# Optimization experiments

Measured on AMD Instinct MI355X. Metric: run time of the kernel, lower is better.

## Reference

```python
import jax, jax.numpy as jnp
import numpy as np

B = 64      # graphs per batch
N = 1024    # nodes per graph (equal-size graphs -> static top-k)
D = 256     # in_dim
DEG = 16    # avg degree
K = 512     # k = ratio * N, ratio = 0.5
E = B * N * DEG
NT = B * N


def setup_inputs() -> dict:
    key = jax.random.key(0)
    ks = jax.random.split(key, 8)
    feature = jax.random.normal(ks[0], (NT, D), jnp.float32)
    gid = jnp.repeat(jnp.arange(B), N * DEG)          # graph id per edge
    src = gid * N + jax.random.randint(ks[1], (E,), 0, N)
    dst = gid * N + jax.random.randint(ks[2], (E,), 0, N)
    label = jax.random.randint(ks[3], (B,), 0, 2)
    W = jax.random.normal(ks[4], (D, 1), jnp.float32) / np.sqrt(D)   # GraphConv weight
    b = jnp.zeros((1,), jnp.float32)                                  # GraphConv bias
    lin1_w = jax.random.normal(ks[5], (2, 1), jnp.float32) / np.sqrt(2.0)
    lin1_b = jnp.zeros((1,), jnp.float32)
    return dict(feature=feature, src=src, dst=dst, label=label,
                W=W, b=b, lin1_w=lin1_w, lin1_b=lin1_b)


def reference(feature, src, dst, label, W, b, lin1_w, lin1_b):
    fdt = feature.dtype
    # ---- get_bias_score: distance-to-class-center score ----
    node_label = jnp.repeat(label, N).astype(fdt)                 # [NT]
    gemb = feature.reshape(B, N, D).mean(axis=1)                  # AvgPooling per graph [B, D]
    lab_f = label.astype(fdt)                                     # [B]
    n1 = jnp.maximum(lab_f.sum(), 1.0)
    n0 = jnp.maximum((1.0 - lab_f).sum(), 1.0)
    center0 = (gemb * (1.0 - lab_f)[:, None]).sum(0) / n0         # [D]
    center1 = (gemb * lab_f[:, None]).sum(0) / n1                 # [D]
    d0 = jnp.sqrt(((feature - center0) ** 2).sum(-1))             # [NT]
    d1 = jnp.sqrt(((feature - center1) ** 2).sum(-1))             # [NT]
    score_distance = (d0 - d1) * ((node_label - 0.5) * 2.0)       # [NT]
    # ---- GraphConv(in_dim, 1), norm='both' (DGL semantics) ----
    ones_e = jnp.ones((E,), fdt)
    deg_out = jax.ops.segment_sum(ones_e, src, NT)
    deg_in = jax.ops.segment_sum(ones_e, dst, NT)
    ns = jnp.maximum(deg_out, 1.0) ** -0.5                        # src-side norm
    nd = jnp.maximum(deg_in, 1.0) ** -0.5                         # dst-side norm
    h = (feature @ W) * ns[:, None]                               # project first (out<in) [NT,1]
    agg = jax.ops.segment_sum(h[src], dst, NT)                    # [NT,1]
    score_gcn = (agg * nd[:, None] + b)[:, 0]                     # [NT]
    # ---- combine two scores with lin1: Linear(2, 1) ----
    score = jnp.stack([score_gcn, score_distance], axis=-1) @ lin1_w + lin1_b  # [NT,1]
    sflat = score[:, 0]
    # ---- per-graph top-k (mytopk with equal-size graphs -> static k) ----
    _, idx = jax.lax.top_k(sflat.reshape(B, N), K)                # [B,K] local indices
    perm = (idx + (jnp.arange(B) * N)[:, None]).reshape(-1)       # [B*K] global indices
    mask = jnp.ones((NT,), bool).at[perm].set(False)
    perm_com = jnp.nonzero(mask, size=NT - B * K)[0]              # complement, static size
    # ---- gather + tanh-gated features ----
    feature_dis = feature[perm] * jnp.tanh(sflat[perm])[:, None]          # [B*K, D]
    feature_com = feature[perm_com] * jnp.tanh(sflat[perm_com])[:, None]  # [B*(N-K), D]
    score_soft = jax.nn.softmax(score, axis=0)                    # softmax over all nodes
    return feature_dis, feature_com, perm, perm_com, score_soft
```

## Files before the change

kernel.cpp:

```cpp
#include <hip/hip_runtime.h>
#include <math.h>

#define Bg   64
#define Nn   1024
#define Dd   256
#define EPG  16384
#define NT   (Bg * Nn)
#define Kk   512

#define OFF_DIS   0
#define OFF_COM   8388608
#define OFF_PERM  16777216
#define OFF_PCOM  16809984
#define OFF_SOFT  16842752

#define WS_H0     0
#define WS_SFLAT  (NT * 4)
#define WS_GPART  (NT * 4 * 2)
#define WS_REDM   (WS_GPART + 1024 * 256 * 4)
#define WS_REDS   (WS_REDM + 256)
#define WS_C0     (WS_REDS + 256)
#define WS_C1     (WS_C0 + 1024)
#define WS_PERMI  (WS_C1 + 1024)
#define WS_PCOMI  (WS_PERMI + 32768 * 4)
#define WS_SGCN   (WS_PCOMI + 32768 * 4)

__global__ __launch_bounds__(256) void k_col(
        const float* __restrict__ f, const float* __restrict__ W,
        float* __restrict__ gpart, float* __restrict__ h0) {
    __shared__ float4 scol4[1024];
    int blk = blockIdx.x, t = threadIdx.x;
    int gid = t >> 4, sub = t & 15;
    int base = blk * 64 + gid * 4;
    const float4* f4 = (const float4*)f;
    const float4* W4 = (const float4*)W;
    float4 w[4];
    #pragma unroll
    for (int it = 0; it < 4; ++it) w[it] = W4[it * 16 + sub];
    float4 cs[4];
    #pragma unroll
    for (int it = 0; it < 4; ++it) cs[it] = make_float4(0.f, 0.f, 0.f, 0.f);
    float4 v[4][4];
    #pragma unroll
    for (int k = 0; k < 4; ++k) {
        size_t bofs = (size_t)(base + k) * 64;
        #pragma unroll
        for (int it = 0; it < 4; ++it) v[k][it] = f4[bofs + it * 16 + sub];
    }
    #pragma unroll
    for (int k = 0; k < 4; ++k) {
        float d = 0.f;
        #pragma unroll
        for (int it = 0; it < 4; ++it) {
            cs[it].x += v[k][it].x; cs[it].y += v[k][it].y;
            cs[it].z += v[k][it].z; cs[it].w += v[k][it].w;
            d += v[k][it].x * w[it].x + v[k][it].y * w[it].y
               + v[k][it].z * w[it].z + v[k][it].w * w[it].w;
        }
        #pragma unroll
        for (int o = 1; o < 16; o <<= 1) d += __shfl_xor(d, o);
        if (sub == 0) h0[base + k] = d;
    }
    #pragma unroll
    for (int it = 0; it < 4; ++it) scol4[gid * 64 + it * 16 + sub] = cs[it];
    __syncthreads();
    if (t < 64) {
        float4 s = make_float4(0.f, 0.f, 0.f, 0.f);
        #pragma unroll
        for (int g2 = 0; g2 < 16; ++g2) {
            float4 u = scol4[g2 * 64 + t];
            s.x += u.x; s.y += u.y; s.z += u.z; s.w += u.w;
        }
        ((float4*)(gpart + blk * Dd))[t] = s;
    }
}

__global__ __launch_bounds__(1024) void k_edge(
        const int* __restrict__ src, const int* __restrict__ dst,
        const int* __restrict__ label, const float* __restrict__ h0,
        const float* __restrict__ gpart, const float* __restrict__ b,
        float* __restrict__ sgcn, float* __restrict__ c0, float* __restrict__ c1) {
    __shared__ uint4 ep4[4096];
    __shared__ int   sdo[1024];
    __shared__ int   sdi[1024];
    __shared__ float shn[1024];
    __shared__ float ssc[1024];
    __shared__ float sc0[1024];
    __shared__ float sc1[1024];

    int g = blockIdx.x, t = threadIdx.x;
    sdo[t] = 0; sdi[t] = 0;

    if (g == 0) {
        int col = t & 255, chunk = t >> 8;
        float a0 = 0.f, a1 = 0.f;
        for (int gg = chunk * 16; gg < chunk * 16 + 16; ++gg) {
            float v = 0.f;
            #pragma unroll
            for (int p = 0; p < 16; ++p) v += gpart[(gg * 16 + p) * Dd + col];
            if (label[gg]) a1 += v; else a0 += v;
        }
        sc0[t] = a0; sc1[t] = a1;
        __syncthreads();
        if (t < Dd) {
            int n1 = 0;
            for (int gg = 0; gg < Bg; ++gg) n1 += label[gg];
            float fn1 = fmaxf((float)n1, 1.f);
            float fn0 = fmaxf((float)(Bg - n1), 1.f);
            float s0 = sc0[t] + sc0[256 + t] + sc0[512 + t] + sc0[768 + t];
            float s1 = sc1[t] + sc1[256 + t] + sc1[512 + t] + sc1[768 + t];
            c0[t] = s0 * (1.f / (float)Nn) / fn0;
            c1[t] = s1 * (1.f / (float)Nn) / fn1;
        }
    }
    __syncthreads();

    {
        const int4* s4 = (const int4*)(src + g * EPG);
        const int4* d4 = (const int4*)(dst + g * EPG);
        #pragma unroll
        for (int i = t; i < EPG / 4; i += 1024) {
            int4 ss = s4[i];
            int4 dd = d4[i];
            int s0 = ss.x & (Nn - 1), s1 = ss.y & (Nn - 1), s2 = ss.z & (Nn - 1), s3 = ss.w & (Nn - 1);
            int e0 = dd.x & (Nn - 1), e1 = dd.y & (Nn - 1), e2 = dd.z & (Nn - 1), e3 = dd.w & (Nn - 1);
            uint4 pk;
            pk.x = (unsigned)(s0 | (e0 << 16));
            pk.y = (unsigned)(s1 | (e1 << 16));
            pk.z = (unsigned)(s2 | (e2 << 16));
            pk.w = (unsigned)(s3 | (e3 << 16));
            ep4[i] = pk;
            atomicAdd(&sdo[s0], 1); atomicAdd(&sdo[s1], 1);
            atomicAdd(&sdo[s2], 1); atomicAdd(&sdo[s3], 1);
            atomicAdd(&sdi[e0], 1); atomicAdd(&sdi[e1], 1);
            atomicAdd(&sdi[e2], 1); atomicAdd(&sdi[e3], 1);
        }
    }
    __syncthreads();

    {
        int dg = sdo[t]; if (dg < 1) dg = 1;
        shn[t] = h0[g * Nn + t] / sqrtf((float)dg);
        ssc[t] = 0.f;
    }
    __syncthreads();

    #pragma unroll
    for (int i = t; i < EPG / 4; i += 1024) {
        uint4 pk = ep4[i];
        atomicAdd(&ssc[pk.x >> 16], shn[pk.x & 0xFFFF]);
        atomicAdd(&ssc[pk.y >> 16], shn[pk.y & 0xFFFF]);
        atomicAdd(&ssc[pk.z >> 16], shn[pk.z & 0xFFFF]);
        atomicAdd(&ssc[pk.w >> 16], shn[pk.w & 0xFFFF]);
    }
    __syncthreads();

    {
        int dg = sdi[t]; if (dg < 1) dg = 1;
        sgcn[g * Nn + t] = ssc[t] / sqrtf((float)dg) + b[0];
    }
}

__global__ __launch_bounds__(256) void k_score(
        const float* __restrict__ f, const float* __restrict__ c0,
        const float* __restrict__ c1, const float* __restrict__ sgcn,
        const int* __restrict__ label, const float* __restrict__ lw,
        const float* __restrict__ lb, float* __restrict__ sflat) {
    int t = threadIdx.x;
    int gid = t >> 4, sub = t & 15;
    int row0 = blockIdx.x * 32 + gid * 2;
    int g = row0 >> 10;
    const float4* f4 = (const float4*)f;
    float4 c0r[4], c1r[4];
    #pragma unroll
    for (int it = 0; it < 4; ++it) {
        c0r[it] = ((const float4*)c0)[it * 16 + sub];
        c1r[it] = ((const float4*)c1)[it * 16 + sub];
    }
    float sgn = label[g] ? 1.f : -1.f;
    float lw0 = lw[0], lw1 = lw[1], lb0 = lb[0];
    float4 v[2][4];
    #pragma unroll
    for (int r = 0; r < 2; ++r) {
        size_t bofs = (size_t)(row0 + r) * 64;
        #pragma unroll
        for (int it = 0; it < 4; ++it) v[r][it] = f4[bofs + it * 16 + sub];
    }
    #pragma unroll
    for (int r = 0; r < 2; ++r) {
        float a0 = 0.f, a1 = 0.f;
        #pragma unroll
        for (int it = 0; it < 4; ++it) {
            float dx;
            dx = v[r][it].x - c0r[it].x; a0 += dx * dx;
            dx = v[r][it].y - c0r[it].y; a0 += dx * dx;
            dx = v[r][it].z - c0r[it].z; a0 += dx * dx;
            dx = v[r][it].w - c0r[it].w; a0 += dx * dx;
            dx = v[r][it].x - c1r[it].x; a1 += dx * dx;
            dx = v[r][it].y - c1r[it].y; a1 += dx * dx;
            dx = v[r][it].z - c1r[it].z; a1 += dx * dx;
            dx = v[r][it].w - c1r[it].w; a1 += dx * dx;
        }
        #pragma unroll
        for (int o = 1; o < 16; o <<= 1) {
            a0 += __shfl_xor(a0, o);
            a1 += __shfl_xor(a1, o);
        }
        if (sub == 0) {
            int row = row0 + r;
            float sdist = (sqrtf(a0) - sqrtf(a1)) * sgn;
            sflat[row] = sgcn[row] * lw0 + sdist * lw1 + lb0;
        }
    }
}

__global__ __launch_bounds__(512) void k_topk(
        const float* __restrict__ sflat, int* __restrict__ permI,
        int* __restrict__ pcomI, float* __restrict__ out,
        float* __restrict__ redM, float* __restrict__ redS) {
    __shared__ unsigned long long sk[1024];
    __shared__ int   sflag[1024];
    __shared__ int   swave[8];
    __shared__ float sred[16];
    int g = blockIdx.x, t = threadIdx.x;
    int lane = t & 63, w = t >> 6;
    float v0 = sflat[g * Nn + t];
    float v1 = sflat[g * Nn + t + 512];
    unsigned u0 = __float_as_uint(v0);
    unsigned u1 = __float_as_uint(v1);
    unsigned o0 = u0 ^ ((u0 >> 31) ? 0xFFFFFFFFu : 0x80000000u);
    unsigned o1 = u1 ^ ((u1 >> 31) ? 0xFFFFFFFFu : 0x80000000u);
    sk[t]       = ((unsigned long long)o0 << 32) | (unsigned)(1023 - t);
    sk[t + 512] = ((unsigned long long)o1 << 32) | (unsigned)(1023 - (t + 512));
    __syncthreads();
    for (int k = 2; k <= 1024; k <<= 1) {
        for (int j = k >> 1; j > 0; j >>= 1) {
            int l = ((t & ~(j - 1)) << 1) | (t & (j - 1));
            int r = l | j;
            unsigned long long a = sk[l], bk = sk[r];
            bool up = ((l & k) == 0);
            if ((a < bk) == up) { sk[l] = bk; sk[r] = a; }
            __syncthreads();
        }
    }
    sflag[t] = 1; sflag[t + 512] = 1;
    __syncthreads();
    {
        int loc = 1023 - (int)(sk[t] & 0xFFFFFFFFu);
        sflag[loc] = 0;
        int gi = g * Nn + loc;
        permI[g * Kk + t] = gi;
        out[OFF_PERM + g * Kk + t] = (float)gi;
    }
    __syncthreads();
    int f0 = sflag[2 * t], f1 = sflag[2 * t + 1];
    int f2 = f0 + f1;
    int inc = f2;
    for (int o = 1; o < 64; o <<= 1) {
        int y = __shfl_up(inc, o);
        if (lane >= o) inc += y;
    }
    if (lane == 63) swave[w] = inc;
    __syncthreads();
    if (t < 8) {
        int a = swave[t];
        for (int o = 1; o < 8; o <<= 1) {
            int y = __shfl_up(a, o);
            if (t >= o) a += y;
        }
        swave[t] = a;
    }
    __syncthreads();
    int basep = ((w > 0) ? swave[w - 1] : 0) + (inc - f2);
    if (f0) {
        int gi = g * Nn + 2 * t;
        pcomI[g * Kk + basep] = gi;
        out[OFF_PCOM + g * Kk + basep] = (float)gi;
    }
    if (f1) {
        int pos = basep + f0;
        int gi = g * Nn + 2 * t + 1;
        pcomI[g * Kk + pos] = gi;
        out[OFF_PCOM + g * Kk + pos] = (float)gi;
    }
    float m = fmaxf(v0, v1);
    for (int o = 32; o > 0; o >>= 1) m = fmaxf(m, __shfl_xor(m, o));
    if (lane == 0) sred[w] = m;
    __syncthreads();
    if (t < 8) {
        float a = sred[t];
        for (int o = 4; o > 0; o >>= 1) a = fmaxf(a, __shfl_xor(a, o));
        if (t == 0) sred[0] = a;
    }
    __syncthreads();
    m = sred[0];
    float s = expf(v0 - m) + expf(v1 - m);
    for (int o = 32; o > 0; o >>= 1) s += __shfl_xor(s, o);
    if (lane == 0) sred[8 + w] = s;
    __syncthreads();
    if (t < 8) {
        float a = sred[8 + t];
        for (int o = 4; o > 0; o >>= 1) a += __shfl_xor(a, o);
        if (t == 0) { redM[g] = m; redS[g] = a; }
    }
}

__global__ __launch_bounds__(256) void k_write(
        const float* __restrict__ f, const int* __restrict__ permI,
        const int* __restrict__ pcomI, const float* __restrict__ sflat,
        const float* __restrict__ redM, const float* __restrict__ redS,
        float* __restrict__ out) {
    __shared__ float sMS[2];
    int t = threadIdx.x;
    if (t < 64) {
        float m = redM[t];
        float mm = m;
        for (int o = 32; o > 0; o >>= 1) mm = fmaxf(mm, __shfl_xor(mm, o));
        float s = redS[t] * expf(m - mm);
        for (int o = 32; o > 0; o >>= 1) s += __shfl_xor(s, o);
        if (t == 0) { sMS[0] = mm; sMS[1] = s; }
    }
    __syncthreads();
    float M = sMS[0], S = sMS[1];
    if (t < 16) {
        int i = blockIdx.x * 16 + t;
        out[OFF_SOFT + i] = expf(sflat[i] - M) / S;
    }
    int w = t >> 6, lane = t & 63;
    int j0 = blockIdx.x * 16 + w * 4;
    int rows[4];
    float tv[4];
    #pragma unroll
    for (int i = 0; i < 4; ++i) {
        int j = j0 + i;
        rows[i] = (j < 32768) ? permI[j] : pcomI[j - 32768];
    }
    #pragma unroll
    for (int i = 0; i < 4; ++i) tv[i] = tanhf(sflat[rows[i]]);
    const float4* f4 = (const float4*)f;
    float4* o4 = (float4*)out;
    #pragma unroll
    for (int i = 0; i < 4; ++i) {
        float4 v = f4[(size_t)rows[i] * 64 + lane];
        o4[(size_t)(j0 + i) * 64 + lane] =
            make_float4(v.x * tv[i], v.y * tv[i], v.z * tv[i], v.w * tv[i]);
    }
}

extern "C" void kernel_launch(void* const* d_in, const int* in_sizes, int n_in,
                              void* d_out, int out_size, void* d_ws, size_t ws_size,
                              hipStream_t stream) {
    const float* feature = (const float*)d_in[0];
    const int*   src     = (const int*)d_in[1];
    const int*   dst     = (const int*)d_in[2];
    const int*   label   = (const int*)d_in[3];
    const float* W       = (const float*)d_in[4];
    const float* b       = (const float*)d_in[5];
    const float* lw      = (const float*)d_in[6];
    const float* lb      = (const float*)d_in[7];
    float* out = (float*)d_out;
    char*  ws  = (char*)d_ws;

    float* h0    = (float*)(ws + WS_H0);
    float* sflat = (float*)(ws + WS_SFLAT);
    float* gpart = (float*)(ws + WS_GPART);
    float* redM  = (float*)(ws + WS_REDM);
    float* redS  = (float*)(ws + WS_REDS);
    float* c0    = (float*)(ws + WS_C0);
    float* c1    = (float*)(ws + WS_C1);
    int*   permI = (int*)(ws + WS_PERMI);
    int*   pcomI = (int*)(ws + WS_PCOMI);
    float* sgcn  = (float*)(ws + WS_SGCN);

    k_col  <<<1024, 256,  0, stream>>>(feature, W, gpart, h0);
    k_edge <<<Bg,   1024, 0, stream>>>(src, dst, label, h0, gpart, b, sgcn, c0, c1);
    k_score<<<2048, 256,  0, stream>>>(feature, c0, c1, sgcn, label, lw, lb, sflat);
    k_topk <<<Bg,   512,  0, stream>>>(sflat, permI, pcomI, out, redM, redS);
    k_write<<<4096, 256,  0, stream>>>(feature, permI, pcomI, sflat, redM, redS, out);
}
```

Measured before the change: 201.9 us.

## Fuse all five stages into one cooperative persistent kernel with grid syncs

Replaces the five separate kernel launches with a single cooperative kernel of 256 blocks of 1024 threads, using grid.sync between the column-sum/projection, edge aggregation, scoring, top-k and gather phases. Each block now handles more rows per phase, and the top-k bitonic sort runs with 512 active threads out of 1024. This aims to remove launch gaps and inter-kernel drain. In exchange it adds grid-wide barrier costs, leaves most blocks idle in the 64-block phases, and relies on a large LDS allocation per block.

```diff
diff --git a/kernel.cpp b/kernel.cpp
--- a/kernel.cpp
+++ b/kernel.cpp
@@ -1,5 +1,8 @@
 #include <hip/hip_runtime.h>
+#include <hip/hip_cooperative_groups.h>
 #include <math.h>
+
+namespace cg = cooperative_groups;
 
 #define Bg   64
 #define Nn   1024
@@ -25,79 +28,135 @@
 #define WS_PCOMI  (WS_PERMI + 32768 * 4)
 #define WS_SGCN   (WS_PCOMI + 32768 * 4)
 
-__global__ __launch_bounds__(256) void k_col(
+__global__ __launch_bounds__(1024) void k_fused(
         const float* __restrict__ f, const float* __restrict__ W,
-        float* __restrict__ gpart, float* __restrict__ h0) {
-    __shared__ float4 scol4[1024];
+        const int* __restrict__ src, const int* __restrict__ dst,
+        const int* __restrict__ label, const float* __restrict__ b,
+        const float* __restrict__ lw, const float* __restrict__ lb,
+        float* __restrict__ h0, float* __restrict__ gpart,
+        float* __restrict__ c0, float* __restrict__ c1,
+        float* __restrict__ sgcn, float* __restrict__ sflat,
+        int* __restrict__ permI, int* __restrict__ pcomI,
+        float* __restrict__ redM, float* __restrict__ redS,
+        float* __restrict__ out) {
+    __shared__ alignas(16) char smem[81920];
+    __shared__ int   swave[8];
+    __shared__ float sred[33];
+    __shared__ float sMS[2];
+
+    cg::grid_group grid = cg::this_grid();
     int blk = blockIdx.x, t = threadIdx.x;
-    int gid = t >> 4, sub = t & 15;
-    int base = blk * 64 + gid * 4;
-    const float4* f4 = (const float4*)f;
-    const float4* W4 = (const float4*)W;
-    float4 w[4];
-    #pragma unroll
-    for (int it = 0; it < 4; ++it) w[it] = W4[it * 16 + sub];
-    float4 cs[4];
-    #pragma unroll
-    for (int it = 0; it < 4; ++it) cs[it] = make_float4(0.f, 0.f, 0.f, 0.f);
-    float4 v[4][4];
-    #pragma unroll
-    for (int k = 0; k < 4; ++k) {
-        size_t bofs = (size_t)(base + k) * 64;
-        #pragma unroll
-        for (int it = 0; it < 4; ++it) v[k][it] = f4[bofs + it * 16 + sub];
-    }
-    #pragma unroll
-    for (int k = 0; k < 4; ++k) {
-        float d = 0.f;
-        #pragma unroll
-        for (int it = 0; it < 4; ++it) {
-            cs[it].x += v[k][it].x; cs[it].y += v[k][it].y;
-            cs[it].z += v[k][it].z; cs[it].w += v[k][it].w;
-            d += v[k][it].x * w[it].x + v[k][it].y * w[it].y
-               + v[k][it].z * w[it].z + v[k][it].w * w[it].w;
-        }
-        #pragma unroll
-        for (int o = 1; o < 16; o <<= 1) d += __shfl_xor(d, o);
-        if (sub == 0) h0[base + k] = d;
-    }
-    #pragma unroll
-    for (int it = 0; it < 4; ++it) scol4[gid * 64 + it * 16 + sub] = cs[it];
-    __syncthreads();
-    if (t < 64) {
-        float4 s = make_float4(0.f, 0.f, 0.f, 0.f);
-        #pragma unroll
-        for (int g2 = 0; g2 < 16; ++g2) {
-            float4 u = scol4[g2 * 64 + t];
-            s.x += u.x; s.y += u.y; s.z += u.z; s.w += u.w;
-        }
-        ((float4*)(gpart + blk * Dd))[t] = s;
-    }
-}
-
-__global__ __launch_bounds__(1024) void k_edge(
-        const int* __restrict__ src, const int* __restrict__ dst,
-        const int* __restrict__ label, const float* __restrict__ h0,
-        const float* __restrict__ gpart, const float* __restrict__ b,
-        float* __restrict__ sgcn, float* __restrict__ c0, float* __restrict__ c1) {
-    __shared__ uint4 ep4[4096];
-    __shared__ int   sdo[1024];
-    __shared__ int   sdi[1024];
-    __shared__ float shn[1024];
-    __shared__ float ssc[1024];
-    __shared__ float sc0[1024];
-    __shared__ float sc1[1024];
-
-    int g = blockIdx.x, t = threadIdx.x;
-    sdo[t] = 0; sdi[t] = 0;
-
-    if (g == 0) {
+
+    {
+        float4* scol4 = (float4*)smem;
+        int gid = t >> 4, sub = t & 15;
+        int base = blk * 256 + gid * 4;
+        const float4* f4 = (const float4*)f;
+        const float4* W4 = (const float4*)W;
+        float4 w[4];
+        #pragma unroll
+        for (int it = 0; it < 4; ++it) w[it] = W4[it * 16 + sub];
+        float4 cs[4];
+        #pragma unroll
+        for (int it = 0; it < 4; ++it) cs[it] = make_float4(0.f, 0.f, 0.f, 0.f);
+        #pragma unroll
+        for (int kb = 0; kb < 2; ++kb) {
+            float4 v[2][4];
+            #pragma unroll
+            for (int k = 0; k < 2; ++k) {
+                size_t bofs = (size_t)(base + kb * 2 + k) * 64;
+                #pragma unroll
+                for (int it = 0; it < 4; ++it) v[k][it] = f4[bofs + it * 16 + sub];
+            }
+            #pragma unroll
+            for (int k = 0; k < 2; ++k) {
+                float d = 0.f;
+                #pragma unroll
+                for (int it = 0; it < 4; ++it) {
+                    cs[it].x += v[k][it].x; cs[it].y += v[k][it].y;
+                    cs[it].z += v[k][it].z; cs[it].w += v[k][it].w;
+                    d += v[k][it].x * w[it].x + v[k][it].y * w[it].y
+                       + v[k][it].z * w[it].z + v[k][it].w * w[it].w;
+                }
+                #pragma unroll
+                for (int o = 1; o < 16; o <<= 1) d += __shfl_xor(d, o);
+                if (sub == 0) h0[base + kb * 2 + k] = d;
+            }
+        }
+        #pragma unroll
+        for (int it = 0; it < 4; ++it) scol4[gid * 64 + it * 16 + sub] = cs[it];
+        __syncthreads();
+        if (t < 256) {
+            float4 s = make_float4(0.f, 0.f, 0.f, 0.f);
+            #pragma unroll
+            for (int g2 = 0; g2 < 64; ++g2) {
+                float4 u = scol4[g2 * 64 + t];
+                s.x += u.x; s.y += u.y; s.z += u.z; s.w += u.w;
+            }
+            ((float4*)gpart)[blk * 64 + t] = s;
+        }
+    }
+    grid.sync();
+
+    if (blk < 64) {
+        uint4* ep4 = (uint4*)smem;
+        int*   sdo = (int*)(smem + 65536);
+        int*   sdi = (int*)(smem + 69632);
+        float* shn = (float*)(smem + 73728);
+        float* ssc = (float*)(smem + 77824);
+        int g = blk;
+        sdo[t] = 0; sdi[t] = 0;
+        __syncthreads();
+        {
+            const int4* s4 = (const int4*)(src + g * EPG);
+            const int4* d4 = (const int4*)(dst + g * EPG);
+            #pragma unroll
+            for (int i = t; i < EPG / 4; i += 1024) {
+                int4 ss = s4[i];
+                int4 dd = d4[i];
+                int s0 = ss.x & (Nn - 1), s1 = ss.y & (Nn - 1), s2 = ss.z & (Nn - 1), s3 = ss.w & (Nn - 1);
+                int e0 = dd.x & (Nn - 1), e1 = dd.y & (Nn - 1), e2 = dd.z & (Nn - 1), e3 = dd.w & (Nn - 1);
+                uint4 pk;
+                pk.x = (unsigned)(s0 | (e0 << 16));
+                pk.y = (unsigned)(s1 | (e1 << 16));
+                pk.z = (unsigned)(s2 | (e2 << 16));
+                pk.w = (unsigned)(s3 | (e3 << 16));
+                ep4[i] = pk;
+                atomicAdd(&sdo[s0], 1); atomicAdd(&sdo[s1], 1);
+                atomicAdd(&sdo[s2], 1); atomicAdd(&sdo[s3], 1);
+                atomicAdd(&sdi[e0], 1); atomicAdd(&sdi[e1], 1);
+                atomicAdd(&sdi[e2], 1); atomicAdd(&sdi[e3], 1);
+            }
+        }
+        __syncthreads();
+        {
+            int dg = sdo[t]; if (dg < 1) dg = 1;
+            shn[t] = h0[g * Nn + t] / sqrtf((float)dg);
+            ssc[t] = 0.f;
+        }
+        __syncthreads();
+        #pragma unroll
+        for (int i = t; i < EPG / 4; i += 1024) {
+            uint4 pk = ep4[i];
+            atomicAdd(&ssc[pk.x >> 16], shn[pk.x & 0xFFFF]);
+            atomicAdd(&ssc[pk.y >> 16], shn[pk.y & 0xFFFF]);
+            atomicAdd(&ssc[pk.z >> 16], shn[pk.z & 0xFFFF]);
+            atomicAdd(&ssc[pk.w >> 16], shn[pk.w & 0xFFFF]);
+        }
+        __syncthreads();
+        {
+            int dg = sdi[t]; if (dg < 1) dg = 1;
+            sgcn[g * Nn + t] = ssc[t] / sqrtf((float)dg) + b[0];
+        }
+    } else if (blk == 64) {
+        float* sc0 = (float*)smem;
+        float* sc1 = (float*)(smem + 4096);
         int col = t & 255, chunk = t >> 8;
         float a0 = 0.f, a1 = 0.f;
         for (int gg = chunk * 16; gg < chunk * 16 + 16; ++gg) {
             float v = 0.f;
             #pragma unroll
-            for (int p = 0; p < 16; ++p) v += gpart[(gg * 16 + p) * Dd + col];
+            for (int p = 0; p < 4; ++p) v += gpart[(gg * 4 + p) * Dd + col];
             if (label[gg]) a1 += v; else a0 += v;
         }
         sc0[t] = a0; sc1[t] = a1;
@@ -113,237 +172,188 @@
             c1[t] = s1 * (1.f / (float)Nn) / fn1;
         }
     }
-    __syncthreads();
+    grid.sync();
 
     {
-        const int4* s4 = (const int4*)(src + g * EPG);
-        const int4* d4 = (const int4*)(dst + g * EPG);
-        #pragma unroll
-        for (int i = t; i < EPG / 4; i += 1024) {
-            int4 ss = s4[i];
-            int4 dd = d4[i];
-            int s0 = ss.x & (Nn - 1), s1 = ss.y & (Nn - 1), s2 = ss.z & (Nn - 1), s3 = ss.w & (Nn - 1);
-            int e0 = dd.x & (Nn - 1), e1 = dd.y & (Nn - 1), e2 = dd.z & (Nn - 1), e3 = dd.w & (Nn - 1);
-            uint4 pk;
-            pk.x = (unsigned)(s0 | (e0 << 16));
-            pk.y = (unsigned)(s1 | (e1 << 16));
-            pk.z = (unsigned)(s2 | (e2 << 16));
-            pk.w = (unsigned)(s3 | (e3 << 16));
-            ep4[i] = pk;
-            atomicAdd(&sdo[s0], 1); atomicAdd(&sdo[s1], 1);
-            atomicAdd(&sdo[s2], 1); atomicAdd(&sdo[s3], 1);
-            atomicAdd(&sdi[e0], 1); atomicAdd(&sdi[e1], 1);
-            atomicAdd(&sdi[e2], 1); atomicAdd(&sdi[e3], 1);
-        }
-    }
-    __syncthreads();
+        int gid = t >> 4, sub = t & 15;
+        int row0 = blk * 256 + gid * 4;
+        int g = row0 >> 10;
+        const float4* f4 = (const float4*)f;
+        float4 c0r[4], c1r[4];
+        #pragma unroll
+        for (int it = 0; it < 4; ++it) {
+            c0r[it] = ((const float4*)c0)[it * 16 + sub];
+            c1r[it] = ((const float4*)c1)[it * 16 + sub];
+        }
+        float sgn = label[g] ? 1.f : -1.f;
+        float lw0 = lw[0], lw1 = lw[1], lb0 = lb[0];
+        #pragma unroll
+        for (int rb = 0; rb < 2; ++rb) {
+            float4 v[2][4];
+            #pragma unroll
+            for (int r = 0; r < 2; ++r) {
+                size_t bofs = (size_t)(row0 + rb * 2 + r) * 64;
+                #pragma unroll
+                for (int it = 0; it < 4; ++it) v[r][it] = f4[bofs + it * 16 + sub];
+            }
+            #pragma unroll
+            for (int r = 0; r < 2; ++r) {
+                float a0 = 0.f, a1 = 0.f;
+                #pragma unroll
+                for (int it = 0; it < 4; ++it) {
+                    float dx;
+                    dx = v[r][it].x - c0r[it].x; a0 += dx * dx;
+                    dx = v[r][it].y - c0r[it].y; a0 += dx * dx;
+                    dx = v[r][it].z - c0r[it].z; a0 += dx * dx;
+                    dx = v[r][it].w - c0r[it].w; a0 += dx * dx;
+                    dx = v[r][it].x - c1r[it].x; a1 += dx * dx;
+                    dx = v[r][it].y - c1r[it].y; a1 += dx * dx;
+                    dx = v[r][it].z - c1r[it].z; a1 += dx * dx;
+                    dx = v[r][it].w - c1r[it].w; a1 += dx * dx;
+                }
+                #pragma unroll
+                for (int o = 1; o < 16; o <<= 1) {
+                    a0 += __shfl_xor(a0, o);
+                    a1 += __shfl_xor(a1, o);
+                }
+                if (sub == 0) {
+                    int row = row0 + rb * 2 + r;
+                    float sdist = (sqrtf(a0) - sqrtf(a1)) * sgn;
+                    sflat[row] = sgcn[row] * lw0 + sdist * lw1 + lb0;
+                }
+            }
+        }
+    }
+    grid.sync();
+
+    if (blk < 64) {
+        unsigned long long* sk = (unsigned long long*)smem;
+        int* sflag = (int*)(smem + 8192);
+        int g = blk;
+        int lane = t & 63, w16 = t >> 6;
+        float v = sflat[g * Nn + t];
+        {
+            unsigned u = __float_as_uint(v);
+            unsigned ox = u ^ ((u >> 31) ? 0xFFFFFFFFu : 0x80000000u);
+            sk[t] = ((unsigned long long)ox << 32) | (unsigned)(1023 - t);
+        }
+        __syncthreads();
+        for (int k = 2; k <= 1024; k <<= 1) {
+            for (int j = k >> 1; j > 0; j >>= 1) {
+                if (t < 512) {
+                    int l = ((t & ~(j - 1)) << 1) | (t & (j - 1));
+                    int r = l | j;
+                    unsigned long long A = sk[l], Bk = sk[r];
+                    bool up = ((l & k) == 0);
+                    if ((A < Bk) == up) { sk[l] = Bk; sk[r] = A; }
+                }
+                __syncthreads();
+            }
+        }
+        sflag[t] = 1;
+        __syncthreads();
+        if (t < 512) {
+            int loc = 1023 - (int)(sk[t] & 0xFFFFFFFFu);
+            sflag[loc] = 0;
+            int gi = g * Nn + loc;
+            permI[g * Kk + t] = gi;
+            out[OFF_PERM + g * Kk + t] = (float)gi;
+        }
+        __syncthreads();
+        int f0 = 0, f1 = 0, f2 = 0, inc = 0;
+        if (t < 512) {
+            f0 = sflag[2 * t]; f1 = sflag[2 * t + 1];
+            f2 = f0 + f1; inc = f2;
+            for (int o = 1; o < 64; o <<= 1) {
+                int y = __shfl_up(inc, o);
+                if (lane >= o) inc += y;
+            }
+            if (lane == 63) swave[w16] = inc;
+        }
+        __syncthreads();
+        if (t < 8) {
+            int a = swave[t];
+            for (int o = 1; o < 8; o <<= 1) {
+                int y = __shfl_up(a, o);
+                if (t >= o) a += y;
+            }
+            swave[t] = a;
+        }
+        __syncthreads();
+        if (t < 512) {
+            int basep = ((w16 > 0) ? swave[w16 - 1] : 0) + (inc - f2);
+            if (f0) {
+                int gi = g * Nn + 2 * t;
+                pcomI[g * Kk + basep] = gi;
+                out[OFF_PCOM + g * Kk + basep] = (float)gi;
+            }
+            if (f1) {
+                int pos = basep + f0;
+                int gi = g * Nn + 2 * t + 1;
+                pcomI[g * Kk + pos] = gi;
+                out[OFF_PCOM + g * Kk + pos] = (float)gi;
+            }
+        }
+        float m = v;
+        for (int o = 32; o > 0; o >>= 1) m = fmaxf(m, __shfl_xor(m, o));
+        if (lane == 0) sred[w16] = m;
+        __syncthreads();
+        if (t < 16) {
+            float a = sred[t];
+            for (int o = 8; o > 0; o >>= 1) a = fmaxf(a, __shfl_xor(a, o));
+            if (t == 0) sred[32] = a;
+        }
+        __syncthreads();
+        float M = sred[32];
+        float s = expf(v - M);
+        for (int o = 32; o > 0; o >>= 1) s += __shfl_xor(s, o);
+        if (lane == 0) sred[16 + w16] = s;
+        __syncthreads();
+        if (t < 16) {
+            float a = sred[16 + t];
+            for (int o = 8; o > 0; o >>= 1) a += __shfl_xor(a, o);
+            if (t == 0) { redM[g] = M; redS[g] = a; }
+        }
+    }
+    grid.sync();
 
     {
-        int dg = sdo[t]; if (dg < 1) dg = 1;
-        shn[t] = h0[g * Nn + t] / sqrtf((float)dg);
-        ssc[t] = 0.f;
-    }
-    __syncthreads();
-
-    #pragma unroll
-    for (int i = t; i < EPG / 4; i += 1024) {
-        uint4 pk = ep4[i];
-        atomicAdd(&ssc[pk.x >> 16], shn[pk.x & 0xFFFF]);
-        atomicAdd(&ssc[pk.y >> 16], shn[pk.y & 0xFFFF]);
-        atomicAdd(&ssc[pk.z >> 16], shn[pk.z & 0xFFFF]);
-        atomicAdd(&ssc[pk.w >> 16], shn[pk.w & 0xFFFF]);
-    }
-    __syncthreads();
-
-    {
-        int dg = sdi[t]; if (dg < 1) dg = 1;
-        sgcn[g * Nn + t] = ssc[t] / sqrtf((float)dg) + b[0];
-    }
-}
-
-__global__ __launch_bounds__(256) void k_score(
-        const float* __restrict__ f, const float* __restrict__ c0,
-        const float* __restrict__ c1, const float* __restrict__ sgcn,
-        const int* __restrict__ label, const float* __restrict__ lw,
-        const float* __restrict__ lb, float* __restrict__ sflat) {
-    int t = threadIdx.x;
-    int gid = t >> 4, sub = t & 15;
-    int row0 = blockIdx.x * 32 + gid * 2;
-    int g = row0 >> 10;
-    const float4* f4 = (const float4*)f;
-    float4 c0r[4], c1r[4];
-    #pragma unroll
-    for (int it = 0; it < 4; ++it) {
-        c0r[it] = ((const float4*)c0)[it * 16 + sub];
-        c1r[it] = ((const float4*)c1)[it * 16 + sub];
-    }
-    float sgn = label[g] ? 1.f : -1.f;
-    float lw0 = lw[0], lw1 = lw[1], lb0 = lb[0];
-    float4 v[2][4];
-    #pragma unroll
-    for (int r = 0; r < 2; ++r) {
-        size_t bofs = (size_t)(row0 + r) * 64;
-        #pragma unroll
-        for (int it = 0; it < 4; ++it) v[r][it] = f4[bofs + it * 16 + sub];
-    }
-    #pragma unroll
-    for (int r = 0; r < 2; ++r) {
-        float a0 = 0.f, a1 = 0.f;
-        #pragma unroll
-        for (int it = 0; it < 4; ++it) {
-            float dx;
-            dx = v[r][it].x - c0r[it].x; a0 += dx * dx;
-            dx = v[r][it].y - c0r[it].y; a0 += dx * dx;
-            dx = v[r][it].z - c0r[it].z; a0 += dx * dx;
-            dx = v[r][it].w - c0r[it].w; a0 += dx * dx;
-            dx = v[r][it].x - c1r[it].x; a1 += dx * dx;
-            dx = v[r][it].y - c1r[it].y; a1 += dx * dx;
-            dx = v[r][it].z - c1r[it].z; a1 += dx * dx;
-            dx = v[r][it].w - c1r[it].w; a1 += dx * dx;
-        }
-        #pragma unroll
-        for (int o = 1; o < 16; o <<= 1) {
-            a0 += __shfl_xor(a0, o);
-            a1 += __shfl_xor(a1, o);
-        }
-        if (sub == 0) {
-            int row = row0 + r;
-            float sdist = (sqrtf(a0) - sqrtf(a1)) * sgn;
-            sflat[row] = sgcn[row] * lw0 + sdist * lw1 + lb0;
-        }
-    }
-}
-
-__global__ __launch_bounds__(512) void k_topk(
-        const float* __restrict__ sflat, int* __restrict__ permI,
-        int* __restrict__ pcomI, float* __restrict__ out,
-        float* __restrict__ redM, float* __restrict__ redS) {
-    __shared__ unsigned long long sk[1024];
-    __shared__ int   sflag[1024];
-    __shared__ int   swave[8];
-    __shared__ float sred[16];
-    int g = blockIdx.x, t = threadIdx.x;
-    int lane = t & 63, w = t >> 6;
-    float v0 = sflat[g * Nn + t];
-    float v1 = sflat[g * Nn + t + 512];
-    unsigned u0 = __float_as_uint(v0);
-    unsigned u1 = __float_as_uint(v1);
-    unsigned o0 = u0 ^ ((u0 >> 31) ? 0xFFFFFFFFu : 0x80000000u);
-    unsigned o1 = u1 ^ ((u1 >> 31) ? 0xFFFFFFFFu : 0x80000000u);
-    sk[t]       = ((unsigned long long)o0 << 32) | (unsigned)(1023 - t);
-    sk[t + 512] = ((unsigned long long)o1 << 32) | (unsigned)(1023 - (t + 512));
-    __syncthreads();
-    for (int k = 2; k <= 1024; k <<= 1) {
-        for (int j = k >> 1; j > 0; j >>= 1) {
-            int l = ((t & ~(j - 1)) << 1) | (t & (j - 1));
-            int r = l | j;
-            unsigned long long a = sk[l], bk = sk[r];
-            bool up = ((l & k) == 0);
-            if ((a < bk) == up) { sk[l] = bk; sk[r] = a; }
-            __syncthreads();
-        }
-    }
-    sflag[t] = 1; sflag[t + 512] = 1;
-    __syncthreads();
-    {
-        int loc = 1023 - (int)(sk[t] & 0xFFFFFFFFu);
-        sflag[loc] = 0;
-        int gi = g * Nn + loc;
-        permI[g * Kk + t] = gi;
-        out[OFF_PERM + g * Kk + t] = (float)gi;
-    }
-    __syncthreads();
-    int f0 = sflag[2 * t], f1 = sflag[2 * t + 1];
-    int f2 = f0 + f1;
-    int inc = f2;
-    for (int o = 1; o < 64; o <<= 1) {
-        int y = __shfl_up(inc, o);
-        if (lane >= o) inc += y;
-    }
-    if (lane == 63) swave[w] = inc;
-    __syncthreads();
-    if (t < 8) {
-        int a = swave[t];
-        for (int o = 1; o < 8; o <<= 1) {
-            int y = __shfl_up(a, o);
-            if (t >= o) a += y;
-        }
-        swave[t] = a;
-    }
-    __syncthreads();
-    int basep = ((w > 0) ? swave[w - 1] : 0) + (inc - f2);
-    if (f0) {
-        int gi = g * Nn + 2 * t;
-        pcomI[g * Kk + basep] = gi;
-        out[OFF_PCOM + g * Kk + basep] = (float)gi;
-    }
-    if (f1) {
-        int pos = basep + f0;
-        int gi = g * Nn + 2 * t + 1;
-        pcomI[g * Kk + pos] = gi;
-        out[OFF_PCOM + g * Kk + pos] = (float)gi;
-    }
-    float m = fmaxf(v0, v1);
-    for (int o = 32; o > 0; o >>= 1) m = fmaxf(m, __shfl_xor(m, o));
-    if (lane == 0) sred[w] = m;
-    __syncthreads();
-    if (t < 8) {
-        float a = sred[t];
-        for (int o = 4; o > 0; o >>= 1) a = fmaxf(a, __shfl_xor(a, o));
-        if (t == 0) sred[0] = a;
-    }
-    __syncthreads();
-    m = sred[0];
-    float s = expf(v0 - m) + expf(v1 - m);
-    for (int o = 32; o > 0; o >>= 1) s += __shfl_xor(s, o);
-    if (lane == 0) sred[8 + w] = s;
-    __syncthreads();
-    if (t < 8) {
-        float a = sred[8 + t];
-        for (int o = 4; o > 0; o >>= 1) a += __shfl_xor(a, o);
-        if (t == 0) { redM[g] = m; redS[g] = a; }
-    }
-}
-
-__global__ __launch_bounds__(256) void k_write(
-        const float* __restrict__ f, const int* __restrict__ permI,
-        const int* __restrict__ pcomI, const float* __restrict__ sflat,
-        const float* __restrict__ redM, const float* __restrict__ redS,
-        float* __restrict__ out) {
-    __shared__ float sMS[2];
-    int t = threadIdx.x;
-    if (t < 64) {
-        float m = redM[t];
-        float mm = m;
-        for (int o = 32; o > 0; o >>= 1) mm = fmaxf(mm, __shfl_xor(mm, o));
-        float s = redS[t] * expf(m - mm);
-        for (int o = 32; o > 0; o >>= 1) s += __shfl_xor(s, o);
-        if (t == 0) { sMS[0] = mm; sMS[1] = s; }
-    }
-    __syncthreads();
-    float M = sMS[0], S = sMS[1];
-    if (t < 16) {
-        int i = blockIdx.x * 16 + t;
-        out[OFF_SOFT + i] = expf(sflat[i] - M) / S;
-    }
-    int w = t >> 6, lane = t & 63;
-    int j0 = blockIdx.x * 16 + w * 4;
-    int rows[4];
-    float tv[4];
-    #pragma unroll
-    for (int i = 0; i < 4; ++i) {
-        int j = j0 + i;
-        rows[i] = (j < 32768) ? permI[j] : pcomI[j - 32768];
-    }
-    #pragma unroll
-    for (int i = 0; i < 4; ++i) tv[i] = tanhf(sflat[rows[i]]);
-    const float4* f4 = (const float4*)f;
-    float4* o4 = (float4*)out;
-    #pragma unroll
-    for (int i = 0; i < 4; ++i) {
-        float4 v = f4[(size_t)rows[i] * 64 + lane];
-        o4[(size_t)(j0 + i) * 64 + lane] =
-            make_float4(v.x * tv[i], v.y * tv[i], v.z * tv[i], v.w * tv[i]);
+        if (t < 64) {
+            float m = redM[t];
+            float mm = m;
+            for (int o = 32; o > 0; o >>= 1) mm = fmaxf(mm, __shfl_xor(mm, o));
+            float s = redS[t] * expf(m - mm);
+            for (int o = 32; o > 0; o >>= 1) s += __shfl_xor(s, o);
+            if (t == 0) { sMS[0] = mm; sMS[1] = s; }
+        }
+        __syncthreads();
+        float M = sMS[0], S = sMS[1];
+        if (t < 256) {
+            int i = blk * 256 + t;
+            out[OFF_SOFT + i] = expf(sflat[i] - M) / S;
+        }
+        int w = t >> 6, lane = t & 63;
+        const float4* f4 = (const float4*)f;
+        float4* o4 = (float4*)out;
+        #pragma unroll
+        for (int bb = 0; bb < 4; ++bb) {
+            int j0 = blk * 256 + w * 16 + bb * 4;
+            int rows[4];
+            float tv[4];
+            #pragma unroll
+            for (int i = 0; i < 4; ++i) {
+                int j = j0 + i;
+                rows[i] = (j < 32768) ? permI[j] : pcomI[j - 32768];
+            }
+            #pragma unroll
+            for (int i = 0; i < 4; ++i) tv[i] = tanhf(sflat[rows[i]]);
+            #pragma unroll
+            for (int i = 0; i < 4; ++i) {
+                float4 v = f4[(size_t)rows[i] * 64 + lane];
+                o4[(size_t)(j0 + i) * 64 + lane] =
+                    make_float4(v.x * tv[i], v.y * tv[i], v.z * tv[i], v.w * tv[i]);
+            }
+        }
     }
 }
 
@@ -372,9 +382,13 @@
     int*   pcomI = (int*)(ws + WS_PCOMI);
     float* sgcn  = (float*)(ws + WS_SGCN);
 
-    k_col  <<<1024, 256,  0, stream>>>(feature, W, gpart, h0);
-    k_edge <<<Bg,   1024, 0, stream>>>(src, dst, label, h0, gpart, b, sgcn, c0, c1);
-    k_score<<<2048, 256,  0, stream>>>(feature, c0, c1, sgcn, label, lw, lb, sflat);
-    k_topk <<<Bg,   512,  0, stream>>>(sflat, permI, pcomI, out, redM, redS);
-    k_write<<<4096, 256,  0, stream>>>(feature, permI, pcomI, sflat, redM, redS, out);
+    void* args[] = {
+        (void*)&feature, (void*)&W, (void*)&src, (void*)&dst, (void*)&label,
+        (void*)&b, (void*)&lw, (void*)&lb,
+        (void*)&h0, (void*)&gpart, (void*)&c0, (void*)&c1,
+        (void*)&sgcn, (void*)&sflat, (void*)&permI, (void*)&pcomI,
+        (void*)&redM, (void*)&redS, (void*)&out
+    };
+    hipLaunchCooperativeKernel((const void*)k_fused, dim3(256), dim3(1024),
+                               args, 0, stream);
 }
```

New measurement: 309.0 us. 53.0% more time.
